# Kernel optimization log

Measured on AMD Instinct MI355X. Metric: run time of the kernel, lower is better.

Reference implementation:

```python
import jax, jax.numpy as jnp
import numpy as np

B, S, IN_DIM, HID, K, NUM_STEPS = 8, 4096, 64, 512, 3, 12


def setup_inputs() -> dict:
    key = jax.random.key(0)
    ks = jax.random.split(key, 7)
    scale_in = 1.0 / np.sqrt(IN_DIM)
    scale_conv = 1.0 / np.sqrt(HID * K)
    scale_out = 1.0 / np.sqrt(HID)
    return {
        "x": jax.random.normal(ks[0], (B, S, IN_DIM), dtype=jnp.float32),
        "W_in": jax.random.normal(ks[1], (IN_DIM, HID), dtype=jnp.float32) * scale_in,
        "b_in": jnp.zeros((HID,), dtype=jnp.float32),
        "W_conv": jax.random.normal(ks[2], (HID, HID, K), dtype=jnp.float32) * scale_conv,
        "b_conv": jnp.zeros((HID,), dtype=jnp.float32),
        "W_out": jax.random.normal(ks[3], (HID, IN_DIM), dtype=jnp.float32) * scale_out,
        "b_out": jnp.zeros((IN_DIM,), dtype=jnp.float32),
    }


def reference(x, W_in, b_in, W_conv, b_conv, W_out, b_out):
    # input projection: (B, S, IN) @ (IN, HID) -> (B, S, HID)
    h = x @ W_in + b_in
    # to channels-first: (B, HID, S)
    h = jnp.transpose(h, (0, 2, 1))
    dn = jax.lax.conv_dimension_numbers(h.shape, W_conv.shape, ("NCH", "OIH", "NCH"))
    pad = K // 2

    def step(h_state, _):
        c = jax.lax.conv_general_dilated(
            h_state, W_conv, window_strides=(1,), padding=[(pad, pad)],
            dimension_numbers=dn)
        c = c + b_conv[None, :, None]
        return jax.nn.relu(c), None

    h, _ = jax.lax.scan(step, h, None, length=NUM_STEPS)
    # back to (B, S, HID), then output projection
    h = jnp.transpose(h, (0, 2, 1))
    return h @ W_out + b_out
```

## Files before the change

### kernel.cpp

```cpp
#include <hip/hip_runtime.h>

#define B_ 8
#define S_ 4096
#define IN_ 64
#define HID_ 512
#define NSTEP 12
#define SP_ (S_ + 2)
#define NP_ (B_ * SP_)
#define NTOT (B_ * S_)

typedef unsigned short u16;
typedef __attribute__((ext_vector_type(8))) short bf16x8;
typedef __attribute__((ext_vector_type(4))) float f32x4;

__device__ __forceinline__ u16 f2bf(float f) {
  unsigned u = __float_as_uint(f);
  u += 0x7fffu + ((u >> 16) & 1u);
  return (u16)(u >> 16);
}

__device__ __forceinline__ void gload16(const void* g, void* l) {
  __builtin_amdgcn_global_load_lds((const __attribute__((address_space(1))) void*)g,
                                   (__attribute__((address_space(3))) void*)l, 16, 0, 0);
}

__global__ void setup_kernel(const float* __restrict__ x, const float* __restrict__ Wc,
                             const float* __restrict__ Wi, const float* __restrict__ Wo,
                             u16* __restrict__ wcb, u16* __restrict__ wib,
                             u16* __restrict__ wob, u16* __restrict__ xbf,
                             u16* __restrict__ h0, u16* __restrict__ h1) {
  const int n_wc = 3 * HID_ * HID_;
  const int n_wio = IN_ * HID_;
  const int n_xb = NTOT * IN_;
  const int n_pad = 2 * B_ * 2 * HID_;
  const long total = (long)n_wc + 2 * n_wio + n_xb + n_pad;
  for (long u = (long)blockIdx.x * blockDim.x + threadIdx.x; u < total;
       u += (long)gridDim.x * blockDim.x) {
    long v = u;
    if (v < n_wc) {
      int k = (int)(v / (HID_ * HID_));
      int rem = (int)(v % (HID_ * HID_));
      int o = rem / HID_, i = rem % HID_;
      wcb[v] = f2bf(Wc[((long)o * HID_ + i) * 3 + k]);
    } else if ((v -= n_wc) < n_wio) {
      int i = (int)(v / IN_), j = (int)(v % IN_);
      wib[v] = f2bf(Wi[j * HID_ + i]);
    } else if ((v -= n_wio) < n_wio) {
      int j = (int)(v / HID_), i = (int)(v % HID_);
      wob[v] = f2bf(Wo[i * IN_ + j]);
    } else if ((v -= n_wio) < n_xb) {
      xbf[v] = f2bf(x[v]);
    } else {
      v -= n_xb;
      int buf = (int)(v / (B_ * 2 * HID_));
      int r = (int)(v % (B_ * 2 * HID_));
      int b = r / (2 * HID_);
      int q = r % (2 * HID_);
      int side = q / HID_, i = q % HID_;
      long p = (long)b * SP_ + (side ? (S_ + 1) : 0);
      (buf ? h1 : h0)[p * HID_ + i] = 0;
    }
  }
}

__global__ __launch_bounds__(256, 2) void proj_in_gemm(const u16* __restrict__ xb,
                                                       const u16* __restrict__ wib,
                                                       const float* __restrict__ bin,
                                                       u16* __restrict__ hout) {
  __shared__ __align__(16) u16 Ab[128 * 64];
  __shared__ __align__(16) u16 Bb[128 * 64];
  const int tid = threadIdx.x, wid = tid >> 6, lane = tid & 63;
  const int nt = blockIdx.x, mt = blockIdx.y;
  const int wr = wid >> 1, wcn = wid & 1, fr = lane & 15, fq = lane >> 4;
#pragma unroll
  for (int c = 0; c < 4; ++c) {
    const int ch = wid * 4 + c;
    const int row = ch * 8 + (lane >> 3), cb = (lane & 7) * 8;
    gload16(wib + (mt * 128 + row) * 64 + cb, &Ab[ch * 512]);
    gload16(xb + ((long)nt * 128 + row) * 64 + cb, &Bb[ch * 512]);
  }
  f32x4 acc[4][4];
#pragma unroll
  for (int m = 0; m < 4; ++m)
#pragma unroll
    for (int n = 0; n < 4; ++n) acc[m][n] = {0.f, 0.f, 0.f, 0.f};
  __syncthreads();
#pragma unroll
  for (int t = 0; t < 2; ++t) {
    const int j0 = t * 32;
    bf16x8 af[4], bfv[4];
#pragma unroll
    for (int m = 0; m < 4; ++m)
      af[m] = *(const bf16x8*)&Ab[(wr * 64 + m * 16 + fr) * 64 + j0 + fq * 8];
#pragma unroll
    for (int n = 0; n < 4; ++n)
      bfv[n] = *(const bf16x8*)&Bb[(wcn * 64 + n * 16 + fr) * 64 + j0 + fq * 8];
#pragma unroll
    for (int m = 0; m < 4; ++m)
#pragma unroll
      for (int n = 0; n < 4; ++n)
        acc[m][n] = __builtin_amdgcn_mfma_f32_16x16x32_bf16(af[m], bfv[n], acc[m][n], 0, 0, 0);
  }
  const int n0 = nt * 128;
  const int bb = n0 / S_, s0v = n0 % S_;
  const int prow = bb * SP_ + s0v + 1;
#pragma unroll
  for (int m = 0; m < 4; ++m) {
    const int i = mt * 128 + wr * 64 + m * 16 + fq * 4;
    const float4 bias = *(const float4*)&bin[i];
#pragma unroll
    for (int n = 0; n < 4; ++n) {
      const int nl = wcn * 64 + n * 16 + fr;
      const long p = prow + nl;
      union { u16 q[4]; uint2 v; } u;
      u.q[0] = f2bf(acc[m][n][0] + bias.x);
      u.q[1] = f2bf(acc[m][n][1] + bias.y);
      u.q[2] = f2bf(acc[m][n][2] + bias.z);
      u.q[3] = f2bf(acc[m][n][3] + bias.w);
      *(uint2*)&hout[p * HID_ + i] = u.v;
    }
  }
}

#define GATE4()                                        \
  asm volatile("s_waitcnt vmcnt(4)" ::: "memory");     \
  __builtin_amdgcn_sched_barrier(0);                   \
  __builtin_amdgcn_s_barrier();                        \
  __builtin_amdgcn_sched_barrier(0);

#define ENDPH()                                        \
  __builtin_amdgcn_sched_barrier(0);                   \
  __builtin_amdgcn_s_barrier();                        \
  __builtin_amdgcn_sched_barrier(0);

#define MFMA16(MB)                                     \
  asm volatile("s_waitcnt lgkmcnt(0)" ::: "memory");   \
  __builtin_amdgcn_sched_barrier(0);                   \
  __builtin_amdgcn_s_setprio(1);                       \
  _Pragma("unroll")                                    \
  for (int mf = 0; mf < 4; ++mf)                       \
    _Pragma("unroll")                                  \
    for (int nf = 0; nf < 4; ++nf)                     \
      acc[(MB) + mf][nf] = __builtin_amdgcn_mfma_f32_16x16x32_bf16(af[mf], bf[nf], acc[(MB) + mf][nf], 0, 0, 0); \
  __builtin_amdgcn_s_setprio(0);                       \
  __builtin_amdgcn_sched_barrier(0);

#define LDA4(BASE, MB, KH)                             \
  _Pragma("unroll")                                    \
  for (int mf = 0; mf < 4; ++mf)                       \
    af[mf] = *(const bf16x8*)((BASE) + (((abase + (KH) * 64) ^ swz) + ((MB) + mf) * 2048));

#define LDB4(BASE, KH)                                 \
  _Pragma("unroll")                                    \
  for (int nf = 0; nf < 4; ++nf)                       \
    bf[nf] = *(const bf16x8*)((BASE) + (((bbase + (KH) * 64) ^ swz) + nf * 2048));

__global__ __launch_bounds__(512, 2) void conv_gemm4(const u16* __restrict__ hin,
                                                     u16* __restrict__ hout,
                                                     const u16* __restrict__ wcb,
                                                     const float* __restrict__ bconv) {
  extern __shared__ __align__(16) u16 smem[];
  const int tid = threadIdx.x;
  const int w = tid >> 6, lane = tid & 63;
  const int wm = w >> 2, wn = w & 3;
  const int fr = lane & 15, fq = lane >> 4;
  const int mbase = blockIdx.y * 256;
  const int n0 = blockIdx.x * 256;
  const int bb = n0 / S_, s0 = n0 % S_;
  const int prow0 = bb * SP_ + s0;

  const int srow = tid >> 3;
  const int scol = (((tid & 7) * 16) ^ (((tid >> 3) & 7) << 4)) >> 1;
  const int wdst = w * 1024;

  auto stage = [&](int d, int u, int r) {
    if (u > 23) u = 23;
    const int kk = u % 3;
    const int i0 = (u / 3) * 64;
    if (r == 0 || r == 3) {
      const int rb = (r == 0) ? 0 : 64;
      char* dst = (char*)smem + d * 32768 + rb * 128;
      const u16* g = wcb + (size_t)kk * (HID_ * HID_) + (size_t)(mbase + rb + srow) * HID_ + i0 + scol;
      gload16(g, dst + wdst);
      gload16(g + 128 * HID_, dst + 16384 + wdst);
    } else {
      const int rb = (r == 1) ? 0 : 128;
      char* dst = (char*)smem + 65536 + d * 32768 + rb * 128;
      const u16* g = hin + (size_t)(prow0 + kk + rb + srow) * HID_ + i0 + scol;
      gload16(g, dst + wdst);
      gload16(g + 64 * HID_, dst + 8192 + wdst);
    }
  };

  f32x4 acc[8][4];
#pragma unroll
  for (int m = 0; m < 8; ++m)
#pragma unroll
    for (int n = 0; n < 4; ++n) acc[m][n] = {0.f, 0.f, 0.f, 0.f};

  stage(0, 0, 0); stage(0, 0, 1); stage(0, 0, 2); stage(0, 0, 3);
  stage(1, 1, 0);

  const int swz = (fr & 7) << 4;
  const int abase = (wm * 128 + fr) * 128 + fq * 16;
  const int bbase = (wn * 64 + fr) * 128 + fq * 16;
  const char* A0 = (const char*)smem;
  const char* A1 = (const char*)smem + 32768;
  const char* B0 = (const char*)smem + 65536;
  const char* B1 = (const char*)smem + 98304;

  for (int j = 0; j < 12; ++j) {
    const int u1 = 2 * j + 1, u2 = 2 * j + 2, u3 = 2 * j + 3;
    bf16x8 af[4], bf[4];

    GATE4();
    LDA4(A0, 0, 0); LDB4(B0, 0);
    stage(1, u1, 1);
    MFMA16(0);
    ENDPH();

    GATE4();
    LDA4(A0, 4, 0);
    stage(1, u1, 2);
    MFMA16(4);
    ENDPH();

    LDA4(A0, 0, 1); LDB4(B0, 1);
    stage(1, u1, 3);
    MFMA16(0);
    ENDPH();

    LDA4(A0, 4, 1);
    stage(0, u2, 0);
    MFMA16(4);
    ENDPH();

    GATE4();
    LDA4(A1, 0, 0); LDB4(B1, 0);
    stage(0, u2, 1);
    MFMA16(0);
    ENDPH();

    GATE4();
    LDA4(A1, 4, 0);
    stage(0, u2, 2);
    MFMA16(4);
    ENDPH();

    LDA4(A1, 0, 1); LDB4(B1, 1);
    stage(0, u2, 3);
    MFMA16(0);
    ENDPH();

    LDA4(A1, 4, 1);
    stage(1, u3, 0);
    MFMA16(4);
    ENDPH();
  }

#pragma unroll
  for (int m = 0; m < 8; ++m) {
    const int o = mbase + wm * 128 + m * 16 + fq * 4;
    const float4 bias = *(const float4*)&bconv[o];
#pragma unroll
    for (int n = 0; n < 4; ++n) {
      const int nl = wn * 64 + n * 16 + fr;
      const long p = (long)prow0 + 1 + nl;
      union { u16 q[4]; uint2 v; } u;
      u.q[0] = f2bf(fmaxf(acc[m][n][0] + bias.x, 0.f));
      u.q[1] = f2bf(fmaxf(acc[m][n][1] + bias.y, 0.f));
      u.q[2] = f2bf(fmaxf(acc[m][n][2] + bias.z, 0.f));
      u.q[3] = f2bf(fmaxf(acc[m][n][3] + bias.w, 0.f));
      *(uint2*)&hout[p * HID_ + o] = u.v;
    }
  }
}

__global__ __launch_bounds__(256, 2) void proj_out_gemm(const u16* __restrict__ hin,
                                                        const u16* __restrict__ wob,
                                                        const float* __restrict__ bout,
                                                        float* __restrict__ out) {
  __shared__ __align__(16) u16 Ab[2][128 * 32];
  __shared__ __align__(16) u16 Bb[2][64 * 32];
  const int tid = threadIdx.x, wid = tid >> 6, lane = tid & 63;
  const int nt = blockIdx.x;
  const int bb = (nt * 128) / S_, s0v = (nt * 128) % S_;
  const int prow0 = bb * SP_ + s0v + 1;
  const int l4 = lane >> 2, lb = (lane & 3) * 8;
  const int fr = lane & 15, fq = lane >> 4;

  f32x4 acc[2][4];
#pragma unroll
  for (int m = 0; m < 2; ++m)
#pragma unroll
    for (int n = 0; n < 4; ++n) acc[m][n] = {0.f, 0.f, 0.f, 0.f};

  auto stage = [&](int buf, int t) {
    const int i0 = t * 32;
#pragma unroll
    for (int c = 0; c < 2; ++c) {
      const int ch = wid * 2 + c;
      gload16(hin + (long)(prow0 + ch * 16 + l4) * HID_ + i0 + lb, &Ab[buf][ch * 512]);
    }
    gload16(wob + (wid * 16 + l4) * HID_ + i0 + lb, &Bb[buf][wid * 512]);
  };

  stage(0, 0);
  __syncthreads();
  for (int t = 0; t < 16; ++t) {
    const int cur = t & 1;
    if (t < 15) stage(cur ^ 1, t + 1);
    bf16x8 af[2], bfv[4];
#pragma unroll
    for (int m = 0; m < 2; ++m)
      af[m] = *(const bf16x8*)&Ab[cur][(wid * 32 + m * 16 + fr) * 32 + fq * 8];
#pragma unroll
    for (int j = 0; j < 4; ++j)
      bfv[j] = *(const bf16x8*)&Bb[cur][(j * 16 + fr) * 32 + fq * 8];
#pragma unroll
    for (int m = 0; m < 2; ++m)
#pragma unroll
      for (int j = 0; j < 4; ++j)
        acc[m][j] = __builtin_amdgcn_mfma_f32_16x16x32_bf16(af[m], bfv[j], acc[m][j], 0, 0, 0);
    __syncthreads();
  }
  const int n0 = nt * 128;
#pragma unroll
  for (int m = 0; m < 2; ++m) {
    const int nbase = n0 + wid * 32 + m * 16 + fq * 4;
#pragma unroll
    for (int jf = 0; jf < 4; ++jf) {
      const int j = jf * 16 + fr;
      const float bj = bout[j];
#pragma unroll
      for (int r = 0; r < 4; ++r)
        out[(long)(nbase + r) * IN_ + j] = acc[m][jf][r] + bj;
    }
  }
}

extern "C" void kernel_launch(void* const* d_in, const int* in_sizes, int n_in,
                              void* d_out, int out_size, void* d_ws, size_t ws_size,
                              hipStream_t stream) {
  (void)in_sizes; (void)n_in; (void)out_size; (void)ws_size;
  const float* x = (const float*)d_in[0];
  const float* W_in = (const float*)d_in[1];
  const float* b_in = (const float*)d_in[2];
  const float* W_conv = (const float*)d_in[3];
  const float* b_conv = (const float*)d_in[4];
  const float* W_out = (const float*)d_in[5];
  const float* b_out = (const float*)d_in[6];
  float* out = (float*)d_out;
  char* ws = (char*)d_ws;

  const size_t hbytes = (size_t)NP_ * HID_ * sizeof(u16);
  u16* h0 = (u16*)ws;
  u16* h1 = (u16*)(ws + hbytes);
  u16* wcb = (u16*)(ws + 2 * hbytes);
  u16* wib = (u16*)(ws + 2 * hbytes + (size_t)3 * HID_ * HID_ * 2);
  u16* wob = (u16*)(ws + 2 * hbytes + ((size_t)3 * HID_ * HID_ + IN_ * HID_) * 2);
  u16* xbf = (u16*)(ws + 2 * hbytes + ((size_t)3 * HID_ * HID_ + 2 * IN_ * HID_) * 2);

  static int lds_attr_set = 0;
  if (!lds_attr_set) {
    (void)hipFuncSetAttribute((const void*)conv_gemm4,
                              hipFuncAttributeMaxDynamicSharedMemorySize, 131072);
    lds_attr_set = 1;
  }

  setup_kernel<<<2048, 256, 0, stream>>>(x, W_conv, W_in, W_out, wcb, wib, wob, xbf, h0, h1);
  proj_in_gemm<<<dim3(NTOT / 128, HID_ / 128), 256, 0, stream>>>(xbf, wib, b_in, h0);
  const u16* cin = h0;
  u16* cout = h1;
  for (int s = 0; s < NSTEP; ++s) {
    conv_gemm4<<<dim3(NTOT / 256, 2), 512, 131072, stream>>>(cin, cout, wcb, b_conv);
    u16* t = (u16*)cin; cin = cout; cout = t;
  }
  proj_out_gemm<<<NTOT / 128, 256, 0, stream>>>(cin, wob, b_out, out);
}
```

Baseline: 582.9 us.

## Restructure conv GEMM phases into an 8-wave ping-pong schedule with relocated barriers

Reorganizes each phase of the conv GEMM main loop. LDS fragment loads and the next global-to-LDS stage are issued first, then a barrier, then the MFMA block, then the vmcnt gate and a closing barrier. The vmcnt waits move from the start of the phase to its end, so the wait for global data overlaps with the MFMAs. The loop is kept rolled (unroll 1) and the LDS address math is simplified with precomputed swizzled column offsets. The barrier reordering changes the hazard timing between LDS buffer reuse and incoming async loads, which could expose races if the gating is wrong.

```diff
diff --git a/kernel.cpp b/kernel.cpp
--- a/kernel.cpp
+++ b/kernel.cpp
@@ -122,40 +122,47 @@
   }
 }
 
-#define GATE4()                                        \
-  asm volatile("s_waitcnt vmcnt(4)" ::: "memory");     \
-  __builtin_amdgcn_sched_barrier(0);                   \
-  __builtin_amdgcn_s_barrier();                        \
-  __builtin_amdgcn_sched_barrier(0);
-
-#define ENDPH()                                        \
-  __builtin_amdgcn_sched_barrier(0);                   \
-  __builtin_amdgcn_s_barrier();                        \
-  __builtin_amdgcn_sched_barrier(0);
-
-#define MFMA16(MB)                                     \
-  asm volatile("s_waitcnt lgkmcnt(0)" ::: "memory");   \
-  __builtin_amdgcn_sched_barrier(0);                   \
-  __builtin_amdgcn_s_setprio(1);                       \
-  _Pragma("unroll")                                    \
-  for (int mf = 0; mf < 4; ++mf)                       \
-    _Pragma("unroll")                                  \
-    for (int nf = 0; nf < 4; ++nf)                     \
-      acc[(MB) + mf][nf] = __builtin_amdgcn_mfma_f32_16x16x32_bf16(af[mf], bf[nf], acc[(MB) + mf][nf], 0, 0, 0); \
-  __builtin_amdgcn_s_setprio(0);                       \
-  __builtin_amdgcn_sched_barrier(0);
-
-#define LDA4(BASE, MB, KH)                             \
-  _Pragma("unroll")                                    \
-  for (int mf = 0; mf < 4; ++mf)                       \
-    af[mf] = *(const bf16x8*)((BASE) + (((abase + (KH) * 64) ^ swz) + ((MB) + mf) * 2048));
-
-#define LDB4(BASE, KH)                                 \
-  _Pragma("unroll")                                    \
-  for (int nf = 0; nf < 4; ++nf)                       \
-    bf[nf] = *(const bf16x8*)((BASE) + (((bbase + (KH) * 64) ^ swz) + nf * 2048));
-
-__global__ __launch_bounds__(512, 2) void conv_gemm4(const u16* __restrict__ hin,
+#define LDA(D, MH, KH) do {                                                     \
+    const char* _p = (const char*)smem + (D) * 32768 + (wm * 2 + (MH)) * 8192   \
+                     + arow + ((KH) ? ck1 : ck0);                               \
+    af[0] = *(const bf16x8*)(_p);                                               \
+    af[1] = *(const bf16x8*)(_p + 2048);                                        \
+    af[2] = *(const bf16x8*)(_p + 4096);                                        \
+    af[3] = *(const bf16x8*)(_p + 6144);                                        \
+  } while (0)
+
+#define LDB(D, KH) do {                                                         \
+    const char* _p = (const char*)smem + 65536 + (D) * 32768 + wn * 8192        \
+                     + arow + ((KH) ? ck1 : ck0);                               \
+    bf[0] = *(const bf16x8*)(_p);                                               \
+    bf[1] = *(const bf16x8*)(_p + 2048);                                        \
+    bf[2] = *(const bf16x8*)(_p + 4096);                                        \
+    bf[3] = *(const bf16x8*)(_p + 6144);                                        \
+  } while (0)
+
+#define MFMA16(MB)                                                              \
+  _Pragma("unroll")                                                             \
+  for (int mf = 0; mf < 4; ++mf)                                                \
+    _Pragma("unroll")                                                           \
+    for (int nf = 0; nf < 4; ++nf)                                              \
+      acc[(MB) + mf][nf] = __builtin_amdgcn_mfma_f32_16x16x32_bf16(af[mf], bf[nf], acc[(MB) + mf][nf], 0, 0, 0)
+
+#define PHASE_TAIL(GATE, MB) do {                                               \
+    __builtin_amdgcn_sched_barrier(0);                                          \
+    __builtin_amdgcn_s_barrier();                                               \
+    asm volatile("s_waitcnt lgkmcnt(0)" ::: "memory");                          \
+    __builtin_amdgcn_sched_barrier(0);                                          \
+    __builtin_amdgcn_s_setprio(1);                                              \
+    MFMA16(MB);                                                                 \
+    __builtin_amdgcn_s_setprio(0);                                              \
+    __builtin_amdgcn_sched_barrier(0);                                          \
+    if (GATE) { asm volatile("s_waitcnt vmcnt(4)" ::: "memory"); }              \
+    __builtin_amdgcn_sched_barrier(0);                                          \
+    __builtin_amdgcn_s_barrier();                                               \
+    __builtin_amdgcn_sched_barrier(0);                                          \
+  } while (0)
+
+__global__ __launch_bounds__(512, 2) void conv_gemm8(const u16* __restrict__ hin,
                                                      u16* __restrict__ hout,
                                                      const u16* __restrict__ wcb,
                                                      const float* __restrict__ bconv) {
@@ -198,64 +205,40 @@
 #pragma unroll
     for (int n = 0; n < 4; ++n) acc[m][n] = {0.f, 0.f, 0.f, 0.f};
 
+  const int swz = (fr & 7) << 4;
+  const int ck0 = (fq * 16) ^ swz;
+  const int ck1 = (64 + fq * 16) ^ swz;
+  const int arow = fr * 128;
+
   stage(0, 0, 0); stage(0, 0, 1); stage(0, 0, 2); stage(0, 0, 3);
   stage(1, 1, 0);
-
-  const int swz = (fr & 7) << 4;
-  const int abase = (wm * 128 + fr) * 128 + fq * 16;
-  const int bbase = (wn * 64 + fr) * 128 + fq * 16;
-  const char* A0 = (const char*)smem;
-  const char* A1 = (const char*)smem + 32768;
-  const char* B0 = (const char*)smem + 65536;
-  const char* B1 = (const char*)smem + 98304;
-
+  asm volatile("s_waitcnt vmcnt(4)" ::: "memory");
+  __builtin_amdgcn_sched_barrier(0);
+  __builtin_amdgcn_s_barrier();
+  __builtin_amdgcn_sched_barrier(0);
+
+  bf16x8 af[4], bf[4];
+
+#pragma unroll 1
   for (int j = 0; j < 12; ++j) {
     const int u1 = 2 * j + 1, u2 = 2 * j + 2, u3 = 2 * j + 3;
-    bf16x8 af[4], bf[4];
-
-    GATE4();
-    LDA4(A0, 0, 0); LDB4(B0, 0);
-    stage(1, u1, 1);
-    MFMA16(0);
-    ENDPH();
-
-    GATE4();
-    LDA4(A0, 4, 0);
-    stage(1, u1, 2);
-    MFMA16(4);
-    ENDPH();
-
-    LDA4(A0, 0, 1); LDB4(B0, 1);
-    stage(1, u1, 3);
-    MFMA16(0);
-    ENDPH();
-
-    LDA4(A0, 4, 1);
-    stage(0, u2, 0);
-    MFMA16(4);
-    ENDPH();
-
-    GATE4();
-    LDA4(A1, 0, 0); LDB4(B1, 0);
-    stage(0, u2, 1);
-    MFMA16(0);
-    ENDPH();
-
-    GATE4();
-    LDA4(A1, 4, 0);
-    stage(0, u2, 2);
-    MFMA16(4);
-    ENDPH();
-
-    LDA4(A1, 0, 1); LDB4(B1, 1);
-    stage(0, u2, 3);
-    MFMA16(0);
-    ENDPH();
-
-    LDA4(A1, 4, 1);
-    stage(1, u3, 0);
-    MFMA16(4);
-    ENDPH();
+
+    LDA(0, 0, 0); LDB(0, 0); stage(1, u1, 1);
+    PHASE_TAIL(1, 0);
+    LDA(0, 1, 0);            stage(1, u1, 2);
+    PHASE_TAIL(0, 4);
+    LDA(0, 0, 1); LDB(0, 1); stage(1, u1, 3);
+    PHASE_TAIL(0, 0);
+    LDA(0, 1, 1);            stage(0, u2, 0);
+    PHASE_TAIL(1, 4);
+    LDA(1, 0, 0); LDB(1, 0); stage(0, u2, 1);
+    PHASE_TAIL(1, 0);
+    LDA(1, 1, 0);            stage(0, u2, 2);
+    PHASE_TAIL(0, 4);
+    LDA(1, 0, 1); LDB(1, 1); stage(0, u2, 3);
+    PHASE_TAIL(0, 0);
+    LDA(1, 1, 1);            stage(1, u3, 0);
+    PHASE_TAIL(1, 4);
   }
 
 #pragma unroll
@@ -363,7 +346,7 @@
 
   static int lds_attr_set = 0;
   if (!lds_attr_set) {
-    (void)hipFuncSetAttribute((const void*)conv_gemm4,
+    (void)hipFuncSetAttribute((const void*)conv_gemm8,
                               hipFuncAttributeMaxDynamicSharedMemorySize, 131072);
     lds_attr_set = 1;
   }
@@ -373,7 +356,7 @@
   const u16* cin = h0;
   u16* cout = h1;
   for (int s = 0; s < NSTEP; ++s) {
-    conv_gemm4<<<dim3(NTOT / 256, 2), 512, 131072, stream>>>(cin, cout, wcb, b_conv);
+    conv_gemm8<<<dim3(NTOT / 256, 2), 512, 131072, stream>>>(cin, cout, wcb, b_conv);
     u16* t = (u16*)cin; cin = cout; cout = t;
   }
   proj_out_gemm<<<NTOT / 128, 256, 0, stream>>>(cin, wob, b_out, out);
```

New measurement: 598.0 us. 1.03x slower.
